# Performance work log

Measured on AMD Instinct MI355X. Metric: run time of the kernel, lower is better.

## Reference

```python
import math
import jax, jax.numpy as jnp
import numpy as np

IN_DIM = 512
OUT_DIM = 512
K = 3
EPS = 1e-8


def setup_inputs() -> dict:
    key = jax.random.key(0)
    k1, k2, k3 = jax.random.split(key, 3)
    b, h, w = 8, 64, 64
    x = jax.random.normal(k1, (b, IN_DIM, h, w), dtype=jnp.float32)
    style = jax.random.normal(k2, (b, IN_DIM), dtype=jnp.float32)
    weight = jax.random.normal(k3, (OUT_DIM, IN_DIM, K, K), dtype=jnp.float32)
    bias = jnp.zeros((OUT_DIM,), dtype=jnp.float32)
    return {"x": x, "style": style, "weight": weight, "bias": bias}


def _mod_weights(weight, style):
    # EqualizedWeight scaling: c = 1/sqrt(prod(shape[1:]))
    c = 1.0 / math.sqrt(IN_DIM * K * K)
    w = weight * c                                    # [out, in, k, k]
    ws = w[None] * (style[:, None, :, None, None] + 1.0)  # [b, out, in, k, k]
    sigma_inv = jax.lax.rsqrt(jnp.sum(ws * ws, axis=(2, 3, 4), keepdims=True) + EPS)
    return ws * sigma_inv


def reference(x, style, weight, bias):
    ws = _mod_weights(weight, style)                  # [b, out, in, k, k]

    def conv_one(xi, wi):
        # xi: [in, h, w], wi: [out, in, k, k]
        y = jax.lax.conv_general_dilated(
            xi[None], wi, window_strides=(1, 1), padding="SAME",
            dimension_numbers=("NCHW", "OIHW", "NCHW"))
        return y[0]

    out = jax.vmap(conv_one)(x, ws)                   # [b, out, h, w]
    return out + bias[None, :, None, None]
```

## Files before the change

### kernel.cpp

```cpp
#include <hip/hip_runtime.h>

#define CIN 512
#define COUT 512
#define HH 64
#define WW 64
#define BB 8
#define KTOT 4608

#define XPD 66
#define BUFSH (4 * 66 * 32)
#define ROWB (66 * 64)

typedef __attribute__((ext_vector_type(8))) short short8;
typedef __attribute__((ext_vector_type(4))) float f32x4;

__device__ inline unsigned short f2bf(float f) {
    unsigned int u = __float_as_uint(f);
    u += 0x7FFFu + ((u >> 16) & 1u);
    return (unsigned short)(u >> 16);
}

__device__ inline void gll16(const void* g, void* l) {
    __builtin_amdgcn_global_load_lds(
        (const __attribute__((address_space(1))) unsigned int*)g,
        (__attribute__((address_space(3))) unsigned int*)l, 16, 0, 0);
}

__global__ __launch_bounds__(256) void zring_kernel(unsigned short* __restrict__ xtp) {
    const int e = blockIdx.x * 256 + threadIdx.x;
    if (e >= BB * 260 * 64) return;
    const int unit = e & 63;
    const int sa = e >> 6;
    const int b = sa / 260;
    const int s = sa - b * 260;
    int yy, xx;
    if (s < 66)       { yy = 0;        xx = s; }
    else if (s < 132) { yy = 65;       xx = s - 66; }
    else if (s < 196) { yy = s - 131;  xx = 0; }
    else              { yy = s - 195;  xx = 65; }
    *(short8*)(xtp + ((size_t)(b * XPD + yy) * XPD + xx) * 512 + unit * 8) =
        (short8){0, 0, 0, 0, 0, 0, 0, 0};
}

__global__ __launch_bounds__(256) void xpose_kernel(const float* __restrict__ x,
                                                    const float* __restrict__ style,
                                                    unsigned short* __restrict__ xtp) {
    __shared__ float tile[32 * 65];
    __shared__ float sst[32];
    const int ic = blockIdx.x;
    const int y  = blockIdx.y;
    const int b  = blockIdx.z;
    const int t  = threadIdx.x;
    if (t < 32) sst[t] = style[b * CIN + ic * 32 + t] + 1.0f;
#pragma unroll
    for (int it = 0; it < 8; ++it) {
        int e = it * 256 + t;
        int ii = e >> 6, xx = e & 63;
        tile[ii * 65 + xx] = x[(((size_t)(b * CIN + ic * 32 + ii) * HH + y) << 6) + xx];
    }
    __syncthreads();
#pragma unroll
    for (int it = 0; it < 8; ++it) {
        int g = it * 256 + t;
        int xx = g >> 5, ii = g & 31;
        xtp[((size_t)(b * XPD + y + 1) * XPD + xx + 1) * 512 + ic * 32 + ii] =
            f2bf(tile[ii * 65 + xx] * sst[ii]);
    }
}

__global__ __launch_bounds__(256) void wpack_kernel(const float* __restrict__ weight,
                                                    unsigned short* __restrict__ wpk) {
    __shared__ float q[KTOT];
    const int o = blockIdx.x;
    const int t = threadIdx.x;
    const float* wrow = weight + (size_t)o * KTOT;
    const float cst = 1.0f / sqrtf((float)KTOT);
#pragma unroll
    for (int it = 0; it < 18; ++it) {
        int e = it * 256 + t;
        q[e] = wrow[e] * cst;
    }
    __syncthreads();
    const int g = o >> 4, l15 = o & 15;
    for (int m = t; m < 576; m += 256) {
        int c   = m / 36;
        int rem = m - c * 36;
        int tap = rem >> 2;
        int l4  = rem & 3;
        short8 v;
#pragma unroll
        for (int e = 0; e < 8; ++e)
            v[e] = (short)f2bf(q[(c * 32 + l4 * 8 + e) * 9 + tap]);
        *(short8*)(wpk + ((((size_t)c * 9 + tap) * 32 + g) * 64 + l4 * 16 + l15) * 8) = v;
    }
}

__global__ __launch_bounds__(256) void sigma_kernel(const float* __restrict__ weight,
                                                    const float* __restrict__ style,
                                                    float* __restrict__ siginv) {
    __shared__ float sred[4][8];
    const int o = blockIdx.x;
    const int t = threadIdx.x;
    const float* wrow = weight + (size_t)o * KTOT;
    float acc[8] = {0.f, 0.f, 0.f, 0.f, 0.f, 0.f, 0.f, 0.f};
#pragma unroll
    for (int ii = 0; ii < 2; ++ii) {
        const int i = t * 2 + ii;
        float wsq = 0.f;
#pragma unroll
        for (int tap = 0; tap < 9; ++tap) {
            float v = wrow[i * 9 + tap];
            wsq += v * v;
        }
#pragma unroll
        for (int b = 0; b < 8; ++b) {
            float s = style[b * CIN + i] + 1.0f;
            acc[b] += wsq * s * s;
        }
    }
#pragma unroll
    for (int b = 0; b < 8; ++b) {
        float v = acc[b];
#pragma unroll
        for (int off = 32; off > 0; off >>= 1) v += __shfl_down(v, off, 64);
        if ((t & 63) == 0) sred[t >> 6][b] = v;
    }
    __syncthreads();
    if (t < 8) {
        const float S = sred[0][t] + sred[1][t] + sred[2][t] + sred[3][t];
        siginv[t * COUT + o] = rsqrtf(S * (1.0f / (float)KTOT) + 1e-8f);
    }
}

__global__ __launch_bounds__(512, 4) void conv_kernel(const unsigned short* __restrict__ wpk,
                                                      const unsigned short* __restrict__ xtp,
                                                      const float* __restrict__ siginv,
                                                      const float* __restrict__ bias,
                                                      float* __restrict__ out) {
    __shared__ __align__(16) unsigned short xs[2 * BUFSH];
    const int bid = blockIdx.x;
    const int k  = bid & 7;
    const int tq = bid >> 3;
    const int ob = k & 1;
    const int b  = (k >> 1) * 2 + (tq >> 5);
    const int yb = tq & 31;
    const int y0 = yb * 2;

    const int tid  = threadIdx.x;
    const int lane = tid & 63;
    const int wid_u = __builtin_amdgcn_readfirstlane(tid >> 6);
    const int l15 = lane & 15, l4 = lane >> 4;
    const int og = wid_u & 3, rp = wid_u >> 2;
    const int g0 = ob * 16 + og * 4;

    const int u = lane & 3;
    const int sl0 = wid_u * 16 + (lane >> 2);
    const int row0 = sl0 / 66, col0 = sl0 - row0 * 66;
    const int sl1 = sl0 + 128;
    const int row1 = sl1 / 66, col1 = sl1 - row1 * 66;
    const int col2 = 58 + (lane >> 2);
    const unsigned short* src0 =
        xtp + ((size_t)(b * XPD + y0 + row0) * XPD + col0) * 512 + (u ^ (col0 & 3)) * 8;
    const unsigned short* src1 =
        xtp + ((size_t)(b * XPD + y0 + row1) * XPD + col1) * 512 + (u ^ (col1 & 3)) * 8;
    const unsigned short* src2 =
        xtp + ((size_t)(b * XPD + y0 + 3) * XPD + col2) * 512 + (u ^ (col2 & 3)) * 8;

    int vB[3];
#pragma unroll
    for (int kx = 0; kx < 3; ++kx)
        vB[kx] = (l15 + kx) * 64 + ((l4 ^ ((l15 + kx) & 3)) * 16);

    f32x4 acc[4][4];
#pragma unroll
    for (int mi = 0; mi < 4; ++mi)
#pragma unroll
        for (int j = 0; j < 4; ++j) acc[mi][j] = (f32x4){0.f, 0.f, 0.f, 0.f};

    const unsigned short* wB = wpk + (size_t)g0 * 512 + lane * 8;

#define STAGE(bufp, icq)                                                                  \
    do {                                                                                  \
        unsigned short* dbase = xs + (bufp) * BUFSH + wid_u * 512;                        \
        gll16(src0 + (size_t)(icq) * 32, dbase);                                          \
        gll16(src1 + (size_t)(icq) * 32, dbase + 4096);                                   \
        if (wid_u == 0 && lane < 32)                                                      \
            gll16(src2 + (size_t)(icq) * 32, xs + (bufp) * BUFSH + 8192);                 \
    } while (0)

#define PHASE(tap, wAc, cbase)                                                            \
    do {                                                                                  \
        short8 afx[4];                                                                    \
        _Pragma("unroll") for (int mi = 0; mi < 4; ++mi)                                  \
            afx[mi] = *(const short8*)((wAc) + (tap) * 16384 + mi * 512);                 \
        short8 bfr[4];                                                                    \
        const char* bp = (const char*)xs + (cbase) +                                      \
                         (rp + (tap) / 3) * ROWB + vB[(tap) % 3];                         \
        _Pragma("unroll") for (int j = 0; j < 4; ++j)                                     \
            bfr[j] = *(const short8*)(bp + j * 1024);                                     \
        __builtin_amdgcn_s_setprio(1);                                                    \
        _Pragma("unroll") for (int mi = 0; mi < 4; ++mi)                                  \
            _Pragma("unroll") for (int j = 0; j < 4; ++j)                                 \
                acc[mi][j] = __builtin_amdgcn_mfma_f32_16x16x32_bf16(                     \
                    afx[mi], bfr[j], acc[mi][j], 0, 0, 0);                                \
        __builtin_amdgcn_s_setprio(0);                                                    \
    } while (0)

    STAGE(0, 0);
    __syncthreads();

#pragma unroll 1
    for (int ic = 0; ic < 16; ++ic) {
        if (ic < 15) STAGE((ic + 1) & 1, ic + 1);
        const unsigned short* wAc = wB + (size_t)ic * (9 * 32 * 512);
        const int cbase = (ic & 1) * (BUFSH * 2);
#pragma unroll
        for (int tap = 0; tap < 9; ++tap) {
            PHASE(tap, wAc, cbase);
        }
        __syncthreads();
    }

    const int yout = y0 + rp;
#pragma unroll
    for (int mi = 0; mi < 4; ++mi) {
        const int obase = ob * 256 + og * 64 + mi * 16 + l4 * 4;
#pragma unroll
        for (int rr = 0; rr < 4; ++rr) {
            const int o = obase + rr;
            const float sv = siginv[b * COUT + o];
            const float bv = bias[o];
            float* orow = out + (((size_t)(b * COUT + o) * HH + yout) << 6);
#pragma unroll
            for (int j = 0; j < 4; ++j) {
                orow[j * 16 + l15] = acc[mi][j][rr] * sv + bv;
            }
        }
    }
#undef STAGE
#undef PHASE
}

extern "C" void kernel_launch(void* const* d_in, const int* in_sizes, int n_in,
                              void* d_out, int out_size, void* d_ws, size_t ws_size,
                              hipStream_t stream) {
    const float* x      = (const float*)d_in[0];
    const float* style  = (const float*)d_in[1];
    const float* weight = (const float*)d_in[2];
    const float* bias   = (const float*)d_in[3];
    float* out = (float*)d_out;

    unsigned short* wpk = (unsigned short*)d_ws;
    unsigned short* xtp = wpk + (size_t)2359296;
    float* siginv = (float*)(xtp + (size_t)BB * XPD * XPD * 512);

    zring_kernel<<<520, 256, 0, stream>>>(xtp);
    xpose_kernel<<<dim3(16, HH, BB), 256, 0, stream>>>(x, style, xtp);
    wpack_kernel<<<COUT, 256, 0, stream>>>(weight, wpk);
    sigma_kernel<<<COUT, 256, 0, stream>>>(weight, style, siginv);
    conv_kernel<<<512, 512, 0, stream>>>(wpk, xtp, siginv, bias, out);
}
```

Before: 167.2 us.

## Double the input-channel chunk per LDS stage to 64 channels

```diff
diff --git a/kernel.cpp b/kernel.cpp
--- a/kernel.cpp
+++ b/kernel.cpp
@@ -8,8 +8,8 @@
 #define KTOT 4608
 
 #define XPD 66
-#define BUFSH (4 * 66 * 32)
-#define ROWB (66 * 64)
+#define BUFSH (4 * 66 * 64)
+#define ROWB (66 * 128)
 
 typedef __attribute__((ext_vector_type(8))) short short8;
 typedef __attribute__((ext_vector_type(4))) float f32x4;
@@ -153,23 +153,25 @@
     const int og = wid_u & 3, rp = wid_u >> 2;
     const int g0 = ob * 16 + og * 4;
 
-    const int u = lane & 3;
-    const int sl0 = wid_u * 16 + (lane >> 2);
-    const int row0 = sl0 / 66, col0 = sl0 - row0 * 66;
-    const int sl1 = sl0 + 128;
-    const int row1 = sl1 / 66, col1 = sl1 - row1 * 66;
-    const int col2 = 58 + (lane >> 2);
-    const unsigned short* src0 =
-        xtp + ((size_t)(b * XPD + y0 + row0) * XPD + col0) * 512 + (u ^ (col0 & 3)) * 8;
-    const unsigned short* src1 =
-        xtp + ((size_t)(b * XPD + y0 + row1) * XPD + col1) * 512 + (u ^ (col1 & 3)) * 8;
-    const unsigned short* src2 =
-        xtp + ((size_t)(b * XPD + y0 + 3) * XPD + col2) * 512 + (u ^ (col2 & 3)) * 8;
-
-    int vB[3];
+    const int up = lane & 7;
+    const unsigned short* srcq[4];
+#pragma unroll
+    for (int t4 = 0; t4 < 4; ++t4) {
+        const int sl = (wid_u + t4 * 8) * 8 + (lane >> 3);
+        const int row = sl / 66, col = sl - row * 66;
+        srcq[t4] = xtp + ((size_t)(b * XPD + y0 + row) * XPD + col) * 512 +
+                   (up ^ (col & 7)) * 8;
+    }
+    const int col4 = 58 + (lane >> 3);
+    const unsigned short* src4 =
+        xtp + ((size_t)(b * XPD + y0 + 3) * XPD + col4) * 512 + (up ^ (col4 & 7)) * 8;
+
+    int vB[3][2];
 #pragma unroll
     for (int kx = 0; kx < 3; ++kx)
-        vB[kx] = (l15 + kx) * 64 + ((l4 ^ ((l15 + kx) & 3)) * 16);
+#pragma unroll
+        for (int ks = 0; ks < 2; ++ks)
+            vB[kx][ks] = (l15 + kx) * 128 + (((ks * 4 + l4) ^ ((l15 + kx) & 7)) * 16);
 
     f32x4 acc[4][4];
 #pragma unroll
@@ -182,22 +184,24 @@
 #define STAGE(bufp, icq)                                                                  \
     do {                                                                                  \
         unsigned short* dbase = xs + (bufp) * BUFSH + wid_u * 512;                        \
-        gll16(src0 + (size_t)(icq) * 32, dbase);                                          \
-        gll16(src1 + (size_t)(icq) * 32, dbase + 4096);                                   \
-        if (wid_u == 0 && lane < 32)                                                      \
-            gll16(src2 + (size_t)(icq) * 32, xs + (bufp) * BUFSH + 8192);                 \
+        gll16(srcq[0] + (size_t)(icq) * 64, dbase);                                       \
+        gll16(srcq[1] + (size_t)(icq) * 64, dbase + 4096);                                \
+        gll16(srcq[2] + (size_t)(icq) * 64, dbase + 8192);                                \
+        gll16(srcq[3] + (size_t)(icq) * 64, dbase + 12288);                               \
+        if (wid_u == 0)                                                                   \
+            gll16(src4 + (size_t)(icq) * 64, xs + (bufp) * BUFSH + 16384);                \
     } while (0)
 
-#define PHASE(tap, wAc, cbase)                                                            \
+#define PHASE(tap, ks, wAc, cbase)                                                        \
     do {                                                                                  \
         short8 afx[4];                                                                    \
         _Pragma("unroll") for (int mi = 0; mi < 4; ++mi)                                  \
-            afx[mi] = *(const short8*)((wAc) + (tap) * 16384 + mi * 512);                 \
+            afx[mi] = *(const short8*)((wAc) + ((ks) * 9 + (tap)) * 16384 + mi * 512);    \
         short8 bfr[4];                                                                    \
         const char* bp = (const char*)xs + (cbase) +                                      \
-                         (rp + (tap) / 3) * ROWB + vB[(tap) % 3];                         \
+                         (rp + (tap) / 3) * ROWB + vB[(tap) % 3][ks];                     \
         _Pragma("unroll") for (int j = 0; j < 4; ++j)                                     \
-            bfr[j] = *(const short8*)(bp + j * 1024);                                     \
+            bfr[j] = *(const short8*)(bp + j * 2048);                                     \
         __builtin_amdgcn_s_setprio(1);                                                    \
         _Pragma("unroll") for (int mi = 0; mi < 4; ++mi)                                  \
             _Pragma("unroll") for (int j = 0; j < 4; ++j)                                 \
@@ -210,13 +214,14 @@
     __syncthreads();
 
 #pragma unroll 1
-    for (int ic = 0; ic < 16; ++ic) {
-        if (ic < 15) STAGE((ic + 1) & 1, ic + 1);
-        const unsigned short* wAc = wB + (size_t)ic * (9 * 32 * 512);
+    for (int ic = 0; ic < 8; ++ic) {
+        if (ic < 7) STAGE((ic + 1) & 1, ic + 1);
+        const unsigned short* wAc = wB + (size_t)ic * (2 * 9 * 32 * 512);
         const int cbase = (ic & 1) * (BUFSH * 2);
 #pragma unroll
         for (int tap = 0; tap < 9; ++tap) {
-            PHASE(tap, wAc, cbase);
+            PHASE(tap, 0, wAc, cbase);
+            PHASE(tap, 1, wAc, cbase);
         }
         __syncthreads();
     }
```

Result: no change. 165.9 us (-0.8%).
